# Kernel tuning notes

Hardware: AMD Instinct MI355X
Metric: run time of the kernel (lower is better)

Reference implementation:

```python
import jax, jax.numpy as jnp
import numpy as np

N_HEAD = 4
D_K = 64
D_V = 64
D_MODEL = 256
LN_EPS = 1e-5


def setup_inputs() -> dict:
    key = jax.random.key(0)
    k1, k2, k3 = jax.random.split(key, 3)
    B, C, H, W = 2, D_MODEL, 64, 64
    q = jax.random.normal(k1, (B, C, H, W), dtype=jnp.float32)
    # w_qkvs: Linear(d_model, n_head*d_k, bias=False), weight [out, in]
    std_qkv = np.sqrt(2.0 / (D_MODEL + D_K))
    w_qkv = jax.random.normal(k2, (N_HEAD * D_K, D_MODEL), dtype=jnp.float32) * std_qkv
    # fc: Linear(n_head*d_v, d_model), xavier-normal-ish init
    std_fc = np.sqrt(2.0 / (N_HEAD * D_V + D_MODEL))
    fc_w = jax.random.normal(k3, (D_MODEL, N_HEAD * D_V), dtype=jnp.float32) * std_fc
    fc_b = jnp.zeros((D_MODEL,), dtype=jnp.float32)
    ln_g = jnp.ones((D_MODEL,), dtype=jnp.float32)
    ln_b = jnp.zeros((D_MODEL,), dtype=jnp.float32)
    return {"q": q, "w_qkv": w_qkv, "fc_w": fc_w, "fc_b": fc_b, "ln_g": ln_g, "ln_b": ln_b}


def reference(q, w_qkv, fc_w, fc_b, ln_g, ln_b):
    B, C, H, W = q.shape
    L = H * W
    # [B, C, H, W] -> [B, L, C]
    x = q.reshape(B, C, L).transpose(0, 2, 1)
    residual = x
    # shared QKV projection (self-attention branch: q == k == v)
    qkv = x @ w_qkv.T                                  # [B, L, nh*dk]
    qh = qkv.reshape(B, L, N_HEAD, D_K).transpose(2, 0, 1, 3)  # [h, B, L, dk]
    scale = jnp.asarray(np.sqrt(D_K), dtype=q.dtype)
    attn = jnp.einsum('hbqd,hbkd->hbqk', qh, qh) / scale       # [h, B, L, L]
    attn = jax.nn.softmax(attn, axis=-1)
    out = jnp.einsum('hbqk,hbkd->hbqd', attn, qh)              # [h, B, L, dv]
    # [h, B, L, dv] -> [B, L, h*dv]
    out = out.transpose(1, 2, 0, 3).reshape(B, L, N_HEAD * D_V)
    out = out @ fc_w.T + fc_b
    out = out + residual
    mu = jnp.mean(out, axis=-1, keepdims=True)
    var = jnp.mean(jnp.square(out - mu), axis=-1, keepdims=True)
    out = (out - mu) / jnp.sqrt(var + LN_EPS) * ln_g + ln_b
    # raw row-major view back to [B, C, H, W] (matches torch .view)
    return out.reshape(B, -1, H, W)
```

## Files before the change

kernel.cpp:

```cpp
#include <hip/hip_runtime.h>

#define L_SEQ 4096
#define DMODEL 256
#define DH 64

typedef __attribute__((ext_vector_type(8))) __bf16 bf16x8;
typedef __attribute__((ext_vector_type(4))) __bf16 bf16v4;
typedef __attribute__((ext_vector_type(8))) __bf16 bf16v8;
typedef __attribute__((ext_vector_type(4))) float f32x4;
typedef __attribute__((ext_vector_type(8))) float f32x8;
typedef __attribute__((ext_vector_type(8))) unsigned short ushort8v;
typedef __attribute__((ext_vector_type(4))) unsigned short ushort4v;

__device__ __forceinline__ float bf2f(unsigned short h) {
  unsigned u = ((unsigned)h) << 16;
  return __builtin_bit_cast(float, u);
}
__device__ __forceinline__ ushort4v cvt4(float a, float b, float c, float d) {
  bf16v4 h = __builtin_convertvector((f32x4){a, b, c, d}, bf16v4);
  return __builtin_bit_cast(ushort4v, h);
}
__device__ __forceinline__ ushort8v cvt8(f32x8 v) {
  bf16v8 h = __builtin_convertvector(v, bf16v8);
  return __builtin_bit_cast(ushort8v, h);
}
__device__ __forceinline__ unsigned short f2bf(float f) {
  __bf16 h = (__bf16)f;
  return __builtin_bit_cast(unsigned short, h);
}
__device__ __forceinline__ bf16x8 ld_frag(const unsigned short* p) {
  return __builtin_bit_cast(bf16x8, *(const ushort8v*)p);
}

__global__ __launch_bounds__(256) void k_transpose(const float* __restrict__ q,
                                                   unsigned short* __restrict__ xbf) {
  __shared__ float T[64 * 65];
  int bx = blockIdx.x;
  int b = bx >> 8, rest = bx & 255;
  int ct = rest >> 6, lt = rest & 63;
  int t = threadIdx.x;
#pragma unroll
  for (int it = 0; it < 4; ++it) {
    int i = (t >> 4) + it * 16;
    int j0 = (t & 15) * 4;
    float4 v = *(const float4*)(q + ((size_t)(b * 256 + ct * 64 + i)) * 4096 + lt * 64 + j0);
    T[i * 65 + j0 + 0] = v.x;
    T[i * 65 + j0 + 1] = v.y;
    T[i * 65 + j0 + 2] = v.z;
    T[i * 65 + j0 + 3] = v.w;
  }
  __syncthreads();
#pragma unroll
  for (int it = 0; it < 2; ++it) {
    int l = (t >> 3) + it * 32;
    int c0 = (t & 7) * 8;
    f32x8 v;
#pragma unroll
    for (int k = 0; k < 8; ++k) v[k] = T[(c0 + k) * 65 + l];
    *(ushort8v*)(xbf + ((size_t)(b * 4096 + lt * 64 + l)) * 256 + ct * 64 + c0) = cvt8(v);
  }
}

#define KP2 136
__global__ __launch_bounds__(256) void k_qkv(const unsigned short* __restrict__ xbf,
                                             const float* __restrict__ w,
                                             unsigned short* __restrict__ Qh,
                                             unsigned short* __restrict__ QhT) {
  __shared__ unsigned short As[64 * KP2];
  __shared__ unsigned short Bs[64 * KP2];
  int bx = blockIdx.x;
  int mtile = bx >> 2, h = bx & 3;
  int m0 = mtile * 64;
  int b = m0 >> 12, l0 = m0 & 4095;
  int t = threadIdx.x;
  int wv = t >> 6, lane = t & 63, g = lane >> 4, ln = lane & 15;
  f32x4 acc[4] = {};
  for (int kb = 0; kb < 2; ++kb) {
#pragma unroll
    for (int it = 0; it < 4; ++it) {
      int idx = t + it * 256;
      int row = idx >> 4;
      int c0 = (idx & 15) * 8;
      *(ushort8v*)(As + row * KP2 + c0) =
          *(const ushort8v*)(xbf + (size_t)(m0 + row) * 256 + kb * 128 + c0);
    }
#pragma unroll
    for (int it = 0; it < 4; ++it) {
      int idx = t + it * 256;
      int row = idx >> 4;
      int c8 = (idx & 15) * 8;
      const float* src = w + (size_t)(h * 64 + row) * 256 + kb * 128 + c8;
      float4 v0 = *(const float4*)(src);
      float4 v1 = *(const float4*)(src + 4);
      *(ushort8v*)(Bs + row * KP2 + c8) =
          cvt8((f32x8){v0.x, v0.y, v0.z, v0.w, v1.x, v1.y, v1.z, v1.w});
    }
    __syncthreads();
#pragma unroll
    for (int kc = 0; kc < 4; ++kc) {
      bf16x8 a = ld_frag(As + (wv * 16 + ln) * KP2 + kc * 32 + g * 8);
#pragma unroll
      for (int tn = 0; tn < 4; ++tn) {
        bf16x8 bb = ld_frag(Bs + (tn * 16 + ln) * KP2 + kc * 32 + g * 8);
        acc[tn] = __builtin_amdgcn_mfma_f32_16x16x32_bf16(a, bb, acc[tn], 0, 0, 0);
      }
    }
    __syncthreads();
  }
  size_t pbase = (size_t)(b * 4 + h);
#pragma unroll
  for (int tn = 0; tn < 4; ++tn) {
#pragma unroll
    for (int r = 0; r < 4; ++r) {
      int lrow = wv * 16 + g * 4 + r;
      int d = tn * 16 + ln;
      unsigned short bv = f2bf(acc[tn][r]);
      As[lrow * 64 + (((d >> 3) ^ (lrow & 7)) * 8) + (d & 7)] = bv;
      Bs[d * 64 + (((lrow >> 3) ^ (d & 7)) * 8) + (lrow & 7)] = bv;
    }
  }
#pragma unroll
  for (int s = 0; s < 2; ++s) {
    int flat = s * 64 + lane;
    int lrow = wv * 16 + (flat >> 3);
    int c8 = lane & 7;
    ushort8v v = *(const ushort8v*)(As + lrow * 64 + ((c8 ^ (lrow & 7)) * 8));
    *(ushort8v*)(Qh + (pbase * L_SEQ + l0 + lrow) * DH + c8 * 8) = v;
  }
  __syncthreads();
#pragma unroll
  for (int s = 0; s < 2; ++s) {
    int flat = s * 256 + t;
    int drow = flat >> 3;
    int c8 = t & 7;
    ushort8v v = *(const ushort8v*)(Bs + drow * 64 + ((c8 ^ (drow & 7)) * 8));
    *(ushort8v*)(QhT + (pbase * DH + drow) * L_SEQ + l0 + c8 * 8) = v;
  }
}

template <int KSPLIT>
__global__ __launch_bounds__(256, 2) void k_attn(const unsigned short* __restrict__ Qh,
                                                 const unsigned short* __restrict__ QhT,
                                                 unsigned short* __restrict__ Opart,
                                                 float* __restrict__ Lpart) {
  const int NKB = 64 / KSPLIT;
  __shared__ unsigned short Kt[64 * 64];
  __shared__ unsigned short Vt[64 * 64];
  __shared__ unsigned short Pb[256 * 64];
  int bx = blockIdx.x;
  int p = bx & 7;
  int u = bx >> 3;
  int qsup = u & 15, ks = u >> 4;
  int t = threadIdx.x;
  int wv = t >> 6, lane = t & 63, g = lane >> 4, ln = lane & 15;
  const unsigned short* Qp = Qh + (size_t)p * L_SEQ * DH;
  const unsigned short* QTp = QhT + (size_t)p * DH * L_SEQ;
  int q0 = qsup * 256;
  int qw = q0 + wv * 64;

  bf16x8 aQ[4][2];
#pragma unroll
  for (int nt = 0; nt < 4; ++nt)
#pragma unroll
    for (int kc = 0; kc < 2; ++kc)
      aQ[nt][kc] = ld_frag(Qp + (size_t)(qw + nt * 16 + ln) * DH + kc * 32 + g * 8);

  const ushort8v ones_u = {0x3F80, 0x3F80, 0x3F80, 0x3F80, 0x3F80, 0x3F80, 0x3F80, 0x3F80};
  const bf16x8 bOnes = __builtin_bit_cast(bf16x8, ones_u);

  f32x4 oacc[4][4] = {};
  f32x4 oaccL[4] = {};

  int srow0 = t >> 3, scol0 = t & 7;
  int srow1 = (t + 256) >> 3, scol1 = (t + 256) & 7;
  int sdst0 = srow0 * 64 + ((scol0 ^ (srow0 & 7)) * 8);
  int sdst1 = srow1 * 64 + ((scol1 ^ (srow1 & 7)) * 8);

  ushort8v kreg0, kreg1, vreg0, vreg1;
  {
    int kbase = (ks * NKB) * 64;
    kreg0 = *(const ushort8v*)(Qp + (size_t)(kbase + srow0) * DH + scol0 * 8);
    kreg1 = *(const ushort8v*)(Qp + (size_t)(kbase + srow1) * DH + scol1 * 8);
    vreg0 = *(const ushort8v*)(QTp + (size_t)srow0 * L_SEQ + kbase + scol0 * 8);
    vreg1 = *(const ushort8v*)(QTp + (size_t)srow1 * L_SEQ + kbase + scol1 * 8);
  }

  for (int kb = 0; kb < NKB; ++kb) {
    __syncthreads();
    *(ushort8v*)(Kt + sdst0) = kreg0;
    *(ushort8v*)(Kt + sdst1) = kreg1;
    *(ushort8v*)(Vt + sdst0) = vreg0;
    *(ushort8v*)(Vt + sdst1) = vreg1;
    __syncthreads();
    if (kb + 1 < NKB) {
      int kbase = (ks * NKB + kb + 1) * 64;
      kreg0 = *(const ushort8v*)(Qp + (size_t)(kbase + srow0) * DH + scol0 * 8);
      kreg1 = *(const ushort8v*)(Qp + (size_t)(kbase + srow1) * DH + scol1 * 8);
      vreg0 = *(const ushort8v*)(QTp + (size_t)srow0 * L_SEQ + kbase + scol0 * 8);
      vreg1 = *(const ushort8v*)(QTp + (size_t)srow1 * L_SEQ + kbase + scol1 * 8);
    }
#pragma unroll
    for (int mt = 0; mt < 4; ++mt) {
      int krow = mt * 16 + ln;
      bf16x8 aK0 = ld_frag(Kt + krow * 64 + (((0 * 4 + g) ^ (ln & 7)) * 8));
      bf16x8 aK1 = ld_frag(Kt + krow * 64 + (((1 * 4 + g) ^ (ln & 7)) * 8));
      f32x4 s[4] = {};
#pragma unroll
      for (int nt = 0; nt < 4; ++nt) {
        s[nt] = __builtin_amdgcn_mfma_f32_16x16x32_bf16(aK0, aQ[nt][0], s[nt], 0, 0, 0);
        s[nt] = __builtin_amdgcn_mfma_f32_16x16x32_bf16(aK1, aQ[nt][1], s[nt], 0, 0, 0);
      }
#pragma unroll
      for (int nt = 0; nt < 4; ++nt) {
        float p0 = __expf(fmaf(s[nt][0], 0.125f, -16.0f));
        float p1 = __expf(fmaf(s[nt][1], 0.125f, -16.0f));
        float p2 = __expf(fmaf(s[nt][2], 0.125f, -16.0f));
        float p3 = __expf(fmaf(s[nt][3], 0.125f, -16.0f));
        ushort4v pk = cvt4(p0, p1, p2, p3);
        int row = wv * 64 + nt * 16 + ln;
        int addr = row * 64 + (((2 * mt + (g >> 1)) ^ (ln & 7)) * 8) + (g & 1) * 4;
        *(ushort4v*)(Pb + addr) = pk;
      }
    }
#pragma unroll
    for (int kc = 0; kc < 2; ++kc) {
      bf16x8 bV[4];
#pragma unroll
      for (int tn = 0; tn < 4; ++tn)
        bV[tn] = ld_frag(Vt + (tn * 16 + ln) * 64 + (((kc * 4 + g) ^ (ln & 7)) * 8));
#pragma unroll
      for (int mq = 0; mq < 4; ++mq) {
        bf16x8 aP = ld_frag(Pb + (wv * 64 + mq * 16 + ln) * 64 + (((kc * 4 + g) ^ (ln & 7)) * 8));
#pragma unroll
        for (int tn = 0; tn < 4; ++tn)
          oacc[mq][tn] = __builtin_amdgcn_mfma_f32_16x16x32_bf16(aP, bV[tn], oacc[mq][tn], 0, 0, 0);
        oaccL[mq] = __builtin_amdgcn_mfma_f32_16x16x32_bf16(aP, bOnes, oaccL[mq], 0, 0, 0);
      }
    }
  }
  size_t pq = (size_t)(ks * 8 + p) * L_SEQ;
  if (ln == 0) {
#pragma unroll
    for (int mq = 0; mq < 4; ++mq)
#pragma unroll
      for (int r = 0; r < 4; ++r)
        __builtin_nontemporal_store(oaccL[mq][r],
                                    &Lpart[pq + qw + mq * 16 + g * 4 + r]);
  }
#pragma unroll
  for (int mq = 0; mq < 4; ++mq) {
#pragma unroll
    for (int r = 0; r < 4; ++r) {
      int row = wv * 64 + mq * 16 + g * 4 + r;
#pragma unroll
      for (int tn = 0; tn < 4; ++tn) {
        int d = tn * 16 + ln;
        Pb[row * 64 + (((d >> 3) ^ (row & 7)) * 8) + (d & 7)] = f2bf(oacc[mq][tn][r]);
      }
    }
  }
#pragma unroll
  for (int s = 0; s < 8; ++s) {
    int flat = s * 64 + lane;
    int row = wv * 64 + (flat >> 3);
    int c8 = lane & 7;
    ushort8v v = *(const ushort8v*)(Pb + row * 64 + ((c8 ^ (row & 7)) * 8));
    __builtin_nontemporal_store(v, (ushort8v*)(Opart + (pq + q0 + row) * DH + c8 * 8));
  }
}

#define CP 72
template <int KSPLIT>
__global__ __launch_bounds__(256) void k_fc(const unsigned short* __restrict__ Opart,
                                            const float* __restrict__ Lpart,
                                            const float* __restrict__ fcw,
                                            const float* __restrict__ qres,
                                            const float* __restrict__ fcb,
                                            const float* __restrict__ lng,
                                            const float* __restrict__ lnb,
                                            float* __restrict__ out) {
  __shared__ unsigned short As[16 * CP];
  __shared__ unsigned short Bs[256 * CP];
  __shared__ float invL[4][16];
  __shared__ float redS[4][16], redQ[4][16], muA[16], rsA[16];
  int bx = blockIdx.x;
  int m0 = bx * 16;
  int b = m0 >> 12, lpart = m0 & 4095;
  int t = threadIdx.x;
  int wv = t >> 6, lane = t & 63, g = lane >> 4, ln = lane & 15;
  if (t < 64) {
    int row = t >> 2, hh = t & 3;
    int p = b * 4 + hh;
    float lsum = 0.f;
#pragma unroll
    for (int ksp = 0; ksp < KSPLIT; ++ksp)
      lsum += Lpart[(size_t)(ksp * 8 + p) * L_SEQ + lpart + row];
    invL[hh][row] = 1.0f / lsum;
  }
  __syncthreads();
  f32x4 acc[4] = {};
  for (int kb = 0; kb < 4; ++kb) {
    if (t < 128) {
      int row = t >> 3, c0 = (t & 7) * 8;
      int qrow = lpart + row;
      int p = b * 4 + kb;
      float inv = invL[kb][row];
      float a8[8] = {0.f, 0.f, 0.f, 0.f, 0.f, 0.f, 0.f, 0.f};
#pragma unroll
      for (int ksp = 0; ksp < KSPLIT; ++ksp) {
        ushort8v v = __builtin_nontemporal_load(
            (const ushort8v*)(Opart + ((size_t)(ksp * 8 + p) * L_SEQ + qrow) * DH + c0));
#pragma unroll
        for (int j = 0; j < 8; ++j) a8[j] += bf2f(v[j]);
      }
      *(ushort8v*)(As + row * CP + c0) =
          cvt8((f32x8){a8[0] * inv, a8[1] * inv, a8[2] * inv, a8[3] * inv,
                       a8[4] * inv, a8[5] * inv, a8[6] * inv, a8[7] * inv});
    }
#pragma unroll
    for (int it = 0; it < 8; ++it) {
      int idx = t + it * 256;
      int row = idx >> 3, c0 = (idx & 7) * 8;
      const float* src = fcw + (size_t)row * 256 + kb * 64 + c0;
      float4 v0 = *(const float4*)(src);
      float4 v1 = *(const float4*)(src + 4);
      *(ushort8v*)(Bs + row * CP + c0) =
          cvt8((f32x8){v0.x, v0.y, v0.z, v0.w, v1.x, v1.y, v1.z, v1.w});
    }
    __syncthreads();
#pragma unroll
    for (int kc = 0; kc < 2; ++kc) {
      bf16x8 a = ld_frag(As + ln * CP + kc * 32 + g * 8);
#pragma unroll
      for (int tn = 0; tn < 4; ++tn) {
        bf16x8 bb = ld_frag(Bs + (wv * 64 + tn * 16 + ln) * CP + kc * 32 + g * 8);
        acc[tn] = __builtin_amdgcn_mfma_f32_16x16x32_bf16(a, bb, acc[tn], 0, 0, 0);
      }
    }
    __syncthreads();
  }
  float fb[4], lg[4], lb[4];
#pragma unroll
  for (int tn = 0; tn < 4; ++tn) {
    int o = wv * 64 + tn * 16 + ln;
    fb[tn] = fcb[o]; lg[tn] = lng[o]; lb[tn] = lnb[o];
  }
  float ps[4] = {0.f, 0.f, 0.f, 0.f}, pq2[4] = {0.f, 0.f, 0.f, 0.f};
#pragma unroll
  for (int tn = 0; tn < 4; ++tn) {
    int o = wv * 64 + tn * 16 + ln;
    float4 res = *(const float4*)(qres + ((size_t)(b * 256 + o)) * 4096 + lpart + g * 4);
    float rv[4] = {res.x, res.y, res.z, res.w};
#pragma unroll
    for (int r = 0; r < 4; ++r) {
      float v = acc[tn][r] + fb[tn] + rv[r];
      acc[tn][r] = v;
      ps[r] += v;
      pq2[r] += v * v;
    }
  }
#pragma unroll
  for (int r = 0; r < 4; ++r) {
    float s = ps[r], q2 = pq2[r];
#pragma unroll
    for (int off = 1; off < 16; off <<= 1) {
      s += __shfl_xor(s, off, 64);
      q2 += __shfl_xor(q2, off, 64);
    }
    if (ln == 0) {
      int row = g * 4 + r;
      redS[wv][row] = s;
      redQ[wv][row] = q2;
    }
  }
  __syncthreads();
  if (t < 16) {
    float s = redS[0][t] + redS[1][t] + redS[2][t] + redS[3][t];
    float q2 = redQ[0][t] + redQ[1][t] + redQ[2][t] + redQ[3][t];
    float mu = s * (1.f / 256.f);
    float var = q2 * (1.f / 256.f) - mu * mu;
    muA[t] = mu;
    rsA[t] = rsqrtf(var + 1e-5f);
  }
  __syncthreads();
#pragma unroll
  for (int r = 0; r < 4; ++r) {
    int row = g * 4 + r;
    float mu = muA[row], rs = rsA[row];
#pragma unroll
    for (int tn = 0; tn < 4; ++tn) {
      int o = wv * 64 + tn * 16 + ln;
      out[(size_t)(m0 + row) * 256 + o] = (acc[tn][r] - mu) * rs * lg[tn] + lb[tn];
    }
  }
}

extern "C" void kernel_launch(void* const* d_in, const int* in_sizes, int n_in,
                              void* d_out, int out_size, void* d_ws, size_t ws_size,
                              hipStream_t stream) {
  const float* q = (const float*)d_in[0];
  const float* w_qkv = (const float*)d_in[1];
  const float* fc_w = (const float*)d_in[2];
  const float* fc_b = (const float*)d_in[3];
  const float* ln_g = (const float*)d_in[4];
  const float* ln_b = (const float*)d_in[5];
  float* out = (float*)d_out;

  unsigned short* Qh = (unsigned short*)d_ws;
  unsigned short* QhT = Qh + 2097152;
  float* Lpart = (float*)(QhT + 2097152);
  unsigned short* Opart = (unsigned short*)((char*)Lpart + 1048576);
  unsigned short* xbf = Opart;

  k_transpose<<<dim3(512), dim3(256), 0, stream>>>(q, xbf);
  k_qkv<<<dim3(512), dim3(256), 0, stream>>>(xbf, w_qkv, Qh, QhT);
  k_attn<4><<<dim3(512), dim3(256), 0, stream>>>(Qh, QhT, Opart, Lpart);
  k_fc<4><<<dim3(512), dim3(256), 0, stream>>>(Opart, Lpart, fc_w, q, fc_b, ln_g, ln_b, out);
}
```

Measured before the change: 141.8 us.

## Load attention K/V fragments directly from global and pre-convert fc weights to bf16

The attention kernel stops staging K and V tiles through shared memory. Each wave now reads its MFMA fragments straight from global memory, which removes two barriers per key block and frees LDS. The trade is redundant global and L2 traffic (all four waves load the same K/V) and no register prefetch to hide that latency. Separately, the fc weight is converted to bf16 once by extra blocks in the transpose kernel, so each fc block no longer re-reads and re-converts the fp32 weights.

```diff
diff --git a/kernel.cpp b/kernel.cpp
--- a/kernel.cpp
+++ b/kernel.cpp
@@ -33,12 +33,20 @@
 }
 
 __global__ __launch_bounds__(256) void k_transpose(const float* __restrict__ q,
-                                                   unsigned short* __restrict__ xbf) {
+                                                   unsigned short* __restrict__ xbf,
+                                                   const float* __restrict__ fcw,
+                                                   unsigned short* __restrict__ fcwbf) {
+  int bx = blockIdx.x;
+  int t = threadIdx.x;
+  if (bx >= 512) {
+    int i = ((bx - 512) * 256 + t) * 4;
+    float4 a = *(const float4*)(fcw + i);
+    *(ushort4v*)(fcwbf + i) = cvt4(a.x, a.y, a.z, a.w);
+    return;
+  }
   __shared__ float T[64 * 65];
-  int bx = blockIdx.x;
   int b = bx >> 8, rest = bx & 255;
   int ct = rest >> 6, lt = rest & 63;
-  int t = threadIdx.x;
 #pragma unroll
   for (int it = 0; it < 4; ++it) {
     int i = (t >> 4) + it * 16;
@@ -144,8 +152,6 @@
                                                  unsigned short* __restrict__ Opart,
                                                  float* __restrict__ Lpart) {
   const int NKB = 64 / KSPLIT;
-  __shared__ unsigned short Kt[64 * 64];
-  __shared__ unsigned short Vt[64 * 64];
   __shared__ unsigned short Pb[256 * 64];
   int bx = blockIdx.x;
   int p = bx & 7;
@@ -171,39 +177,14 @@
   f32x4 oacc[4][4] = {};
   f32x4 oaccL[4] = {};
 
-  int srow0 = t >> 3, scol0 = t & 7;
-  int srow1 = (t + 256) >> 3, scol1 = (t + 256) & 7;
-  int sdst0 = srow0 * 64 + ((scol0 ^ (srow0 & 7)) * 8);
-  int sdst1 = srow1 * 64 + ((scol1 ^ (srow1 & 7)) * 8);
-
-  ushort8v kreg0, kreg1, vreg0, vreg1;
-  {
-    int kbase = (ks * NKB) * 64;
-    kreg0 = *(const ushort8v*)(Qp + (size_t)(kbase + srow0) * DH + scol0 * 8);
-    kreg1 = *(const ushort8v*)(Qp + (size_t)(kbase + srow1) * DH + scol1 * 8);
-    vreg0 = *(const ushort8v*)(QTp + (size_t)srow0 * L_SEQ + kbase + scol0 * 8);
-    vreg1 = *(const ushort8v*)(QTp + (size_t)srow1 * L_SEQ + kbase + scol1 * 8);
-  }
-
+  int kbase0 = ks * NKB * 64;
   for (int kb = 0; kb < NKB; ++kb) {
-    __syncthreads();
-    *(ushort8v*)(Kt + sdst0) = kreg0;
-    *(ushort8v*)(Kt + sdst1) = kreg1;
-    *(ushort8v*)(Vt + sdst0) = vreg0;
-    *(ushort8v*)(Vt + sdst1) = vreg1;
-    __syncthreads();
-    if (kb + 1 < NKB) {
-      int kbase = (ks * NKB + kb + 1) * 64;
-      kreg0 = *(const ushort8v*)(Qp + (size_t)(kbase + srow0) * DH + scol0 * 8);
-      kreg1 = *(const ushort8v*)(Qp + (size_t)(kbase + srow1) * DH + scol1 * 8);
-      vreg0 = *(const ushort8v*)(QTp + (size_t)srow0 * L_SEQ + kbase + scol0 * 8);
-      vreg1 = *(const ushort8v*)(QTp + (size_t)srow1 * L_SEQ + kbase + scol1 * 8);
-    }
+    int key0 = kbase0 + kb * 64;
 #pragma unroll
     for (int mt = 0; mt < 4; ++mt) {
-      int krow = mt * 16 + ln;
-      bf16x8 aK0 = ld_frag(Kt + krow * 64 + (((0 * 4 + g) ^ (ln & 7)) * 8));
-      bf16x8 aK1 = ld_frag(Kt + krow * 64 + (((1 * 4 + g) ^ (ln & 7)) * 8));
+      const unsigned short* kp = Qp + (size_t)(key0 + mt * 16 + ln) * DH + g * 8;
+      bf16x8 aK0 = ld_frag(kp);
+      bf16x8 aK1 = ld_frag(kp + 32);
       f32x4 s[4] = {};
 #pragma unroll
       for (int nt = 0; nt < 4; ++nt) {
@@ -227,7 +208,7 @@
       bf16x8 bV[4];
 #pragma unroll
       for (int tn = 0; tn < 4; ++tn)
-        bV[tn] = ld_frag(Vt + (tn * 16 + ln) * 64 + (((kc * 4 + g) ^ (ln & 7)) * 8));
+        bV[tn] = ld_frag(QTp + (size_t)(tn * 16 + ln) * L_SEQ + key0 + kc * 32 + g * 8);
 #pragma unroll
       for (int mq = 0; mq < 4; ++mq) {
         bf16x8 aP = ld_frag(Pb + (wv * 64 + mq * 16 + ln) * 64 + (((kc * 4 + g) ^ (ln & 7)) * 8));
@@ -273,7 +254,7 @@
 template <int KSPLIT>
 __global__ __launch_bounds__(256) void k_fc(const unsigned short* __restrict__ Opart,
                                             const float* __restrict__ Lpart,
-                                            const float* __restrict__ fcw,
+                                            const unsigned short* __restrict__ fcwbf,
                                             const float* __restrict__ qres,
                                             const float* __restrict__ fcb,
                                             const float* __restrict__ lng,
@@ -321,11 +302,8 @@
     for (int it = 0; it < 8; ++it) {
       int idx = t + it * 256;
       int row = idx >> 3, c0 = (idx & 7) * 8;
-      const float* src = fcw + (size_t)row * 256 + kb * 64 + c0;
-      float4 v0 = *(const float4*)(src);
-      float4 v1 = *(const float4*)(src + 4);
       *(ushort8v*)(Bs + row * CP + c0) =
-          cvt8((f32x8){v0.x, v0.y, v0.z, v0.w, v1.x, v1.y, v1.z, v1.w});
+          *(const ushort8v*)(fcwbf + (size_t)row * 256 + kb * 64 + c0);
     }
     __syncthreads();
 #pragma unroll
@@ -410,10 +388,11 @@
   unsigned short* QhT = Qh + 2097152;
   float* Lpart = (float*)(QhT + 2097152);
   unsigned short* Opart = (unsigned short*)((char*)Lpart + 1048576);
+  unsigned short* fcwbf = Opart + (size_t)4 * 8 * 4096 * 64;
   unsigned short* xbf = Opart;
 
-  k_transpose<<<dim3(512), dim3(256), 0, stream>>>(q, xbf);
+  k_transpose<<<dim3(576), dim3(256), 0, stream>>>(q, xbf, fc_w, fcwbf);
   k_qkv<<<dim3(512), dim3(256), 0, stream>>>(xbf, w_qkv, Qh, QhT);
   k_attn<4><<<dim3(512), dim3(256), 0, stream>>>(Qh, QhT, Opart, Lpart);
-  k_fc<4><<<dim3(512), dim3(256), 0, stream>>>(Opart, Lpart, fc_w, q, fc_b, ln_g, ln_b, out);
-}
+  k_fc<4><<<dim3(512), dim3(256), 0, stream>>>(Opart, Lpart, fcwbf, q, fc_b, ln_g, ln_b, out);
+}
```

Result: slower. 152.4 us (+7.5%).
